# Performance work log

Measured on AMD Instinct MI355X. Metric: run time of the kernel, lower is better.

## Reference

```python
import jax, jax.numpy as jnp
import numpy as np
import math

B, F, N, EMB, H, NC, L = 16, 60, 512, 128, 4, 27, 2
EPS = 1e-5


def _ln(x, g, b):
    m = x.mean(-1, keepdims=True)
    v = ((x - m) ** 2).mean(-1, keepdims=True)
    return (x - m) / jnp.sqrt(v + EPS) * g + b


def _bn(x, g, b):
    # BatchNorm1d in training mode: batch statistics over dim 0
    m = x.mean(0)
    v = ((x - m) ** 2).mean(0)
    return (x - m) / jnp.sqrt(v + EPS) * g + b


def _pos_encoding(S, D):
    pos = jnp.arange(S, dtype=jnp.float32)[:, None]
    div = jnp.exp(jnp.arange(0, D, 2, dtype=jnp.float32) * (-math.log(10000.0) / D))
    ang = pos * div  # [S, D/2]
    return jnp.stack([jnp.sin(ang), jnp.cos(ang)], axis=-1).reshape(S, D)


def setup_inputs():
    key = jax.random.key(0)
    ks = jax.random.split(key, 16)
    rn = lambda i, shape, s: (jax.random.normal(ks[i], shape) * s).astype(jnp.float32)
    z = lambda *shape: jnp.zeros(shape, jnp.float32)
    o = lambda *shape: jnp.ones(shape, jnp.float32)
    return {
        "x": jax.random.normal(ks[0], (B, F, N, 3), dtype=jnp.float32),
        "frame_length": jax.random.randint(ks[1], (B,), 1, F + 1, dtype=jnp.int32),
        # PointNet encoder (shared per-point MLP 3->64->128->EMB, max-pool)
        "enc_w1": rn(2, (3, 64), 0.3), "enc_b1": z(64),
        "enc_w2": rn(3, (64, 128), 0.1), "enc_b2": z(128),
        "enc_w3": rn(4, (128, EMB), 0.1), "enc_b3": z(EMB),
        "cls_token": rn(5, (1, 1, EMB), 0.02), "cls_pos": rn(6, (1, 1, EMB), 0.02),
        # 2-layer post-norm TransformerEncoder (d=128, h=4, ff=256)
        "in_w": rn(7, (L, 3 * EMB, EMB), 0.05), "in_b": z(L, 3 * EMB),
        "out_w": rn(8, (L, EMB, EMB), 0.05), "out_b": z(L, EMB),
        "ln1_g": o(L, EMB), "ln1_b": z(L, EMB),
        "ff1_w": rn(9, (L, 256, EMB), 0.05), "ff1_b": z(L, 256),
        "ff2_w": rn(10, (L, EMB, 256), 0.05), "ff2_b": z(L, EMB),
        "ln2_g": o(L, EMB), "ln2_b": z(L, EMB),
        # MLP head (weights stored [in, out])
        "fc1_w": rn(11, (2 * EMB, 128), 0.05), "fc1_b": z(128),
        "bn1_g": o(128), "bn1_b": z(128),
        "fc15_w": rn(12, (128, 64), 0.05), "fc15_b": z(64),
        "bn15_g": o(64), "bn15_b": z(64),
        "fc2_w": rn(13, (64, 32), 0.05), "fc2_b": z(32),
        "bn2_g": o(32), "bn2_b": z(32),
        "fc_w": rn(14, (32, NC), 0.05), "fc_b": z(NC),
    }


def _forward(x, frame_length, enc_w1, enc_b1, enc_w2, enc_b2, enc_w3, enc_b3,
             cls_token, cls_pos, in_w, in_b, out_w, out_b, ln1_g, ln1_b,
             ff1_w, ff1_b, ff2_w, ff2_b, ln2_g, ln2_b,
             fc1_w, fc1_b, bn1_g, bn1_b, fc15_w, fc15_b, bn15_g, bn15_b,
             fc2_w, fc2_b, bn2_g, bn2_b, fc_w, fc_b):
    dh = EMB // H
    # --- per-frame PointNet encoder, vectorized over (B, F) ---
    # (replaces the ragged Python loop; padded frames are masked to zero below,
    #  exactly matching y = zeros(...) filled only for valid frames)
    h = jax.nn.relu(jnp.einsum('bfnc,cd->bfnd', x, enc_w1) + enc_b1)
    h = jax.nn.relu(h @ enc_w2 + enc_b2)
    h = h @ enc_w3 + enc_b3
    y = h.max(axis=2)  # [B, F, EMB]
    valid = (jnp.arange(F)[None, :] < frame_length[:, None])  # [B, F]
    y = jnp.where(valid[..., None], y, 0.0)

    # --- cls token + sinusoidal positions ---
    pe = _pos_encoding(F, EMB)[None]  # [1, F, EMB]
    y = jnp.concatenate([jnp.broadcast_to(cls_token, (B, 1, EMB)), y], axis=1)
    pos = jnp.concatenate([cls_pos, pe], axis=1)
    y = y + pos  # [B, F+1, EMB]

    S = F + 1
    kpm = jnp.arange(S)[None, :] >= (frame_length + 1)[:, None]  # True = pad
    bias = jnp.where(kpm, -1e9, 0.0)[:, None, None, :]  # [B,1,1,S]

    for l in range(L):
        qkv = y @ in_w[l].T + in_b[l]  # [B,S,3*EMB]
        q, k, v = jnp.split(qkv, 3, axis=-1)
        q = q.reshape(B, S, H, dh).transpose(0, 2, 1, 3)
        k = k.reshape(B, S, H, dh).transpose(0, 2, 1, 3)
        v = v.reshape(B, S, H, dh).transpose(0, 2, 1, 3)
        scores = jnp.einsum('bhqd,bhkd->bhqk', q, k) / math.sqrt(dh) + bias
        attn = jax.nn.softmax(scores, axis=-1)
        o = jnp.einsum('bhqk,bhkd->bhqd', attn, v).transpose(0, 2, 1, 3).reshape(B, S, EMB)
        y = _ln(y + (o @ out_w[l].T + out_b[l]), ln1_g[l], ln1_b[l])
        ff = jax.nn.relu(y @ ff1_w[l].T + ff1_b[l]) @ ff2_w[l].T + ff2_b[l]
        y = _ln(y + ff, ln2_g[l], ln2_b[l])

    # --- ragged gather: cls output + last valid frame output ---
    z1 = y[:, 0, :]
    z2 = y[jnp.arange(B), frame_length]  # position frame_length[i] (cls offset)
    zc = jnp.concatenate([z1, z2], axis=1)  # [B, 2*EMB]

    lrelu = lambda t: jax.nn.leaky_relu(t, negative_slope=0.2)
    y1 = lrelu(_bn(zc @ fc1_w + fc1_b, bn1_g, bn1_b))
    y1 = lrelu(_bn(y1 @ fc15_w + fc15_b, bn15_g, bn15_b))
    y1 = lrelu(_bn(y1 @ fc2_w + fc2_b, bn2_g, bn2_b))
    return y1 @ fc_w + fc_b  # [B, NC]


def reference(x, frame_length, enc_w1, enc_b1, enc_w2, enc_b2, enc_w3, enc_b3,
              cls_token, cls_pos, in_w, in_b, out_w, out_b, ln1_g, ln1_b,
              ff1_w, ff1_b, ff2_w, ff2_b, ln2_g, ln2_b,
              fc1_w, fc1_b, bn1_g, bn1_b, fc15_w, fc15_b, bn15_g, bn15_b,
              fc2_w, fc2_b, bn2_g, bn2_b, fc_w, fc_b):
    return _forward(x, frame_length, enc_w1, enc_b1, enc_w2, enc_b2, enc_w3, enc_b3,
                    cls_token, cls_pos, in_w, in_b, out_w, out_b, ln1_g, ln1_b,
                    ff1_w, ff1_b, ff2_w, ff2_b, ln2_g, ln2_b,
                    fc1_w, fc1_b, bn1_g, bn1_b, fc15_w, fc15_b, bn15_g, bn15_b,
                    fc2_w, fc2_b, bn2_g, bn2_b, fc_w, fc_b)
```

## Files before the change

### kernel.cpp

```cpp
#include <hip/hip_runtime.h>
#include <math.h>

#define SS 61
#define EPSV 1e-5f

typedef __attribute__((ext_vector_type(8))) short bf16x8;
typedef __attribute__((ext_vector_type(4))) short s16x4;
typedef __attribute__((ext_vector_type(4))) float f32x4;

__device__ __forceinline__ short f2bf(float f){
  return __builtin_bit_cast(short, (__bf16)f);
}
__device__ __forceinline__ float bf2f(short s){
  unsigned u = ((unsigned)(unsigned short)s) << 16;
  return __builtin_bit_cast(float, u);
}
__device__ __forceinline__ bf16x8 pack8(f32x4 lo, f32x4 hi){
  bf16x8 r;
  r[0]=f2bf(lo[0]); r[1]=f2bf(lo[1]); r[2]=f2bf(lo[2]); r[3]=f2bf(lo[3]);
  r[4]=f2bf(hi[0]); r[5]=f2bf(hi[1]); r[6]=f2bf(hi[2]); r[7]=f2bf(hi[3]);
  return r;
}
__device__ __forceinline__ s16x4 pack4(f32x4 v){
  s16x4 r; r[0]=f2bf(v[0]); r[1]=f2bf(v[1]); r[2]=f2bf(v[2]); r[3]=f2bf(v[3]); return r;
}
#define YI(t,d) (((t)<<7) + ((d) ^ (((t)&7)<<2)))
#define OI(t,e) (((t)<<7) + ((e) ^ (((t)&7)<<2)))
#define FI(t,e) (((t)<<8) + ((e) ^ (((t)&7)<<2)))
#define VI(k,d) (((k)<<5) + ((d) ^ (((k)&7)<<2)))

__global__ __launch_bounds__(256) void prep_kernel(
    const float* __restrict__ ew1, const float* __restrict__ eb1,
    const float* __restrict__ ew2, const float* __restrict__ ew3,
    const float* __restrict__ in_w, const float* __restrict__ ow,
    const float* __restrict__ f1w, const float* __restrict__ f2w,
    const float* __restrict__ fc1w, const float* __restrict__ fc15w,
    const float* __restrict__ fc2w, const float* __restrict__ fcw,
    unsigned short* __restrict__ wbf)
{
  int s = blockIdx.x * 256 + threadIdx.x;
  int i = s & 7, lane = (s >> 3) & 63, frag = s >> 9;
  int c = lane & 15, g = lane >> 4;
  int sig = 16 * (i >> 2) + 4 * g + (i & 3);
  unsigned short outv;
  if (frag < 8) {
    int mt = frag & 3;
    float base = (sig < 3) ? ew1[sig * 64 + 16 * mt + c]
               : (sig == 3 ? eb1[16 * mt + c] : 0.f);
    short hv = f2bf(base);
    if (frag < 4) outv = (unsigned short)hv;
    else { float rv = base - bf2f(hv); outv = (unsigned short)f2bf(rv); }
  } else if (frag < 24) {
    int f = frag - 8; int mt = f >> 1, ks = f & 1;
    outv = (unsigned short)f2bf(ew2[(32 * ks + sig) * 128 + 16 * mt + c]);
  } else if (frag < 56) {
    int f = frag - 24; int mt = f >> 2, ks = f & 3;
    outv = (unsigned short)f2bf(ew3[(32 * ks + sig) * 128 + 16 * mt + c]);
  } else if (frag < 568) {
    int f = frag - 56; int l = f >> 8; f &= 255;
    float v;
    if (f < 96) { int tq = f >> 2, ks = f & 3;
      v = in_w[(size_t)l * 49152 + (size_t)(16 * tq + c) * 128 + 32 * ks + sig]; }
    else if (f < 128) { int f3 = f - 96; int t = f3 >> 2, ks = f3 & 3;
      v = ow[(size_t)l * 16384 + (size_t)(16 * t + c) * 128 + 32 * ks + sig]; }
    else if (f < 192) { int f3 = f - 128; int t = f3 >> 2, ks = f3 & 3;
      v = f1w[(size_t)l * 32768 + (size_t)(16 * t + c) * 128 + 32 * ks + sig]; }
    else { int f3 = f - 192; int t = f3 >> 3, ks = f3 & 7;
      v = f2w[(size_t)l * 32768 + (size_t)(16 * t + c) * 256 + 32 * ks + sig]; }
    outv = (unsigned short)f2bf(v);
  } else {
    int f = frag - 568;
    float v; int hl;
    if (f < 128) { hl = f >> 6; int f6 = f & 63; int mt = f6 >> 3, ks = f6 & 7;
      v = fc1w[(32 * ks + sig) * 128 + 16 * mt + c]; }
    else if (f < 160) { int f2_ = f - 128; hl = f2_ >> 4; int f4 = f2_ & 15; int mt = f4 >> 2, ks = f4 & 3;
      v = fc15w[(32 * ks + sig) * 64 + 16 * mt + c]; }
    else if (f < 168) { int f2_ = f - 160; hl = f2_ >> 2; int f4 = f2_ & 3; int mt = f4 >> 1, ks = f4 & 1;
      v = fc2w[(32 * ks + sig) * 32 + 16 * mt + c]; }
    else { int f2_ = f - 168; hl = f2_ >> 1; int mt = f2_ & 1; int m = 16 * mt + c;
      v = (m < 27) ? fcw[sig * 27 + m] : 0.f; }
    short hv = f2bf(v);
    outv = hl ? (unsigned short)f2bf(v - bf2f(hv)) : (unsigned short)hv;
  }
  wbf[s] = outv;
}

__global__ __launch_bounds__(256, 1) void enc_kernel(
    const float* __restrict__ x,
    const float* __restrict__ eb2, const float* __restrict__ eb3,
    const unsigned short* __restrict__ wbf,
    float* __restrict__ ymax)
{
  const int tid = threadIdx.x, lane = tid & 63, wv = tid >> 6;
  const int c = lane & 15, g = lane >> 4;
  const int frame = blockIdx.x * 4 + wv;
  const bf16x8* wf = (const bf16x8*)wbf;

  bf16x8 A1h[4], A1l[4];
#pragma unroll
  for (int mt = 0; mt < 4; mt++) { A1h[mt] = wf[mt * 64 + lane]; A1l[mt] = wf[(4 + mt) * 64 + lane]; }
  bf16x8 A2f[8][2];
#pragma unroll
  for (int mt = 0; mt < 8; mt++)
#pragma unroll
    for (int ks = 0; ks < 2; ks++) A2f[mt][ks] = wf[(8 + mt * 2 + ks) * 64 + lane];
  bf16x8 A3f[8][4];
#pragma unroll
  for (int mt = 0; mt < 8; mt++)
#pragma unroll
    for (int ks = 0; ks < 4; ks++) A3f[mt][ks] = wf[(24 + mt * 4 + ks) * 64 + lane];
  f32x4 b2v[8];
#pragma unroll
  for (int mt = 0; mt < 8; mt++) b2v[mt] = *(const f32x4*)(eb2 + 16 * mt + 4 * g);

  f32x4 pool[8];
#pragma unroll
  for (int mt = 0; mt < 8; mt++) pool[mt] = {-1e30f, -1e30f, -1e30f, -1e30f};

  const float* xf = x + (size_t)frame * 1536;
  float nx[2][3];
#pragma unroll
  for (int nt = 0; nt < 2; nt++) {
    const float* xp = xf + (16 * nt + c) * 3;
    nx[nt][0] = xp[0]; nx[nt][1] = xp[1]; nx[nt][2] = xp[2];
  }

  for (int t = 0; t < 16; t++) {
    float cx[2][3];
#pragma unroll
    for (int nt = 0; nt < 2; nt++) {
      cx[nt][0] = nx[nt][0]; cx[nt][1] = nx[nt][1]; cx[nt][2] = nx[nt][2];
    }
    if (t < 15) {
#pragma unroll
      for (int nt = 0; nt < 2; nt++) {
        const float* xp = xf + ((t + 1) * 32 + 16 * nt + c) * 3;
        nx[nt][0] = xp[0]; nx[nt][1] = xp[1]; nx[nt][2] = xp[2];
      }
    }
#pragma unroll
    for (int nt = 0; nt < 2; nt++) {
      bf16x8 bxh = {0,0,0,0,0,0,0,0}, bxl = {0,0,0,0,0,0,0,0};
      if (g == 0) {
        short h0 = f2bf(cx[nt][0]), h1_ = f2bf(cx[nt][1]), h2_ = f2bf(cx[nt][2]);
        bxh[0] = h0; bxh[1] = h1_; bxh[2] = h2_; bxh[3] = (short)0x3F80;
        bxl[0] = f2bf(cx[nt][0] - bf2f(h0));
        bxl[1] = f2bf(cx[nt][1] - bf2f(h1_));
        bxl[2] = f2bf(cx[nt][2] - bf2f(h2_));
      }
      f32x4 d1[4];
#pragma unroll
      for (int mt = 0; mt < 4; mt++) {
        f32x4 a = {0.f, 0.f, 0.f, 0.f};
        a = __builtin_amdgcn_mfma_f32_16x16x32_bf16(A1h[mt], bxh, a, 0, 0, 0);
        a = __builtin_amdgcn_mfma_f32_16x16x32_bf16(A1h[mt], bxl, a, 0, 0, 0);
        a = __builtin_amdgcn_mfma_f32_16x16x32_bf16(A1l[mt], bxh, a, 0, 0, 0);
        d1[mt] = a;
      }
      bf16x8 B2[2];
#pragma unroll
      for (int ks = 0; ks < 2; ks++) {
        bf16x8 r;
#pragma unroll
        for (int i = 0; i < 8; i++)
          r[i] = f2bf(fmaxf(d1[2 * ks + (i >> 2)][i & 3], 0.f));
        B2[ks] = r;
      }
      f32x4 acc2[8];
#pragma unroll
      for (int mt = 0; mt < 8; mt++) {
        f32x4 a = b2v[mt];
        a = __builtin_amdgcn_mfma_f32_16x16x32_bf16(A2f[mt][0], B2[0], a, 0, 0, 0);
        a = __builtin_amdgcn_mfma_f32_16x16x32_bf16(A2f[mt][1], B2[1], a, 0, 0, 0);
        acc2[mt] = a;
      }
      bf16x8 B3[4];
#pragma unroll
      for (int ks = 0; ks < 4; ks++) {
        bf16x8 r;
#pragma unroll
        for (int i = 0; i < 8; i++)
          r[i] = f2bf(fmaxf(acc2[2 * ks + (i >> 2)][i & 3], 0.f));
        B3[ks] = r;
      }
#pragma unroll
      for (int mt = 0; mt < 8; mt++) {
        f32x4 a = {0.f, 0.f, 0.f, 0.f};
        a = __builtin_amdgcn_mfma_f32_16x16x32_bf16(A3f[mt][0], B3[0], a, 0, 0, 0);
        a = __builtin_amdgcn_mfma_f32_16x16x32_bf16(A3f[mt][1], B3[1], a, 0, 0, 0);
        a = __builtin_amdgcn_mfma_f32_16x16x32_bf16(A3f[mt][2], B3[2], a, 0, 0, 0);
        a = __builtin_amdgcn_mfma_f32_16x16x32_bf16(A3f[mt][3], B3[3], a, 0, 0, 0);
#pragma unroll
        for (int r = 0; r < 4; r++) pool[mt][r] = fmaxf(pool[mt][r], a[r]);
      }
    }
  }

#pragma unroll
  for (int mt = 0; mt < 8; mt++)
#pragma unroll
    for (int r = 0; r < 4; r++) {
      float v = pool[mt][r];
      v = fmaxf(v, __shfl_xor(v, 1, 64));
      v = fmaxf(v, __shfl_xor(v, 2, 64));
      v = fmaxf(v, __shfl_xor(v, 4, 64));
      v = fmaxf(v, __shfl_xor(v, 8, 64));
      pool[mt][r] = v;
    }
  if (c == 0) {
#pragma unroll
    for (int mt = 0; mt < 8; mt++)
#pragma unroll
      for (int r = 0; r < 4; r++) {
        const int ch = 16 * mt + 4 * g + r;
        ymax[(size_t)frame * 128 + ch] = pool[mt][r] + eb3[ch];
      }
  }
}

__global__ __launch_bounds__(512, 1) void xformer_kernel(
    const float* __restrict__ ymax, const int* __restrict__ fl,
    const float* __restrict__ ctok, const float* __restrict__ cpos,
    const unsigned short* __restrict__ wbf,
    const float* __restrict__ in_b, const float* __restrict__ ob,
    const float* __restrict__ l1g, const float* __restrict__ l1b,
    const float* __restrict__ f1b, const float* __restrict__ f2b,
    const float* __restrict__ l2g, const float* __restrict__ l2b,
    float* __restrict__ zbuf)
{
  __shared__ __align__(16) float ylds[64 * 128];
  __shared__ __align__(16) unsigned short ubuf[64 * 256];
  __shared__ __align__(16) unsigned short kq4[2][8][4][64][4];
  const int b = blockIdx.x, tid = threadIdx.x;
  const int w8 = tid >> 6, lane = tid & 63, c = lane & 15, g = lane >> 4;
  const int h = w8 >> 1, sub = w8 & 1;
  const int flb = fl[b];
  const float scl = 0.17677669529663687f;

  for (int it = 0; it < 16; it++) {
    int idx = it * 512 + tid;
    int t = idx >> 7, d = idx & 127;
    float v;
    if (t == 0) v = ctok[d] + cpos[d];
    else if (t <= 60) {
      int f = t - 1;
      float ym = (f < flb) ? ymax[(size_t)(b * 60 + f) * 128 + d] : 0.f;
      float dv = __expf((float)(d & ~1) * (-0.07195578416f));
      float ang = (float)f * dv;
      v = ym + ((d & 1) ? __cosf(ang) : __sinf(ang));
    } else v = 0.f;
    ylds[YI(t, d)] = v;
  }
  __syncthreads();

  for (int l = 0; l < 2; l++) {
    const unsigned short* WL = wbf + 28672 + (size_t)l * 131072;
    const bf16x8* wq  = (const bf16x8*)WL;
    const bf16x8* wo  = (const bf16x8*)(WL + 49152);
    const bf16x8* w1p = (const bf16x8*)(WL + 65536);
    const bf16x8* w2p = (const bf16x8*)(WL + 98304);
    unsigned short* vb = ubuf + 8192 + h * 2048;

    {
      bf16x8 yB[4][4];
#pragma unroll
      for (int nt = 0; nt < 4; nt++)
#pragma unroll
        for (int ks = 0; ks < 4; ks++) {
          f32x4 lo = *(const f32x4*)&ylds[YI(16 * nt + c, 32 * ks + 4 * g)];
          f32x4 hi = *(const f32x4*)&ylds[YI(16 * nt + c, 32 * ks + 16 + 4 * g)];
          yB[nt][ks] = pack8(lo, hi);
        }
#pragma unroll
      for (int p = 0; p < 3; p++) {
        const int tq = p * 8 + w8;
        bf16x8 Af[4];
#pragma unroll
        for (int ks = 0; ks < 4; ks++) Af[ks] = wq[(tq * 4 + ks) * 64 + lane];
        f32x4 bias = *(const f32x4*)(in_b + l * 384 + p * 128 + 16 * w8 + 4 * g);
        f32x4 acc[4];
#pragma unroll
        for (int nt = 0; nt < 4; nt++) acc[nt] = bias;
#pragma unroll
        for (int ks = 0; ks < 4; ks++)
#pragma unroll
          for (int nt = 0; nt < 4; nt++)
            acc[nt] = __builtin_amdgcn_mfma_f32_16x16x32_bf16(Af[ks], yB[nt][ks], acc[nt], 0, 0, 0);
        if (p == 2) {
#pragma unroll
          for (int nt = 0; nt < 4; nt++)
            *(s16x4*)&vb[VI(16 * nt + c, 16 * sub + 4 * g)] = pack4(acc[nt]);
        } else {
#pragma unroll
          for (int nt = 0; nt < 4; nt++) {
            f32x4 sv = acc[nt];
            if (p == 0) sv = sv * scl;
            *(s16x4*)&kq4[p][w8][nt][lane][0] = pack4(sv);
          }
        }
      }
    }
    __syncthreads();

    {
      bf16x8 Ak[4], Bq2[2];
#pragma unroll
      for (int kt = 0; kt < 4; kt++) {
        s16x4 lo = *(const s16x4*)&kq4[1][2 * h][kt][lane][0];
        s16x4 hi = *(const s16x4*)&kq4[1][2 * h + 1][kt][lane][0];
        Ak[kt] = __builtin_shufflevector(lo, hi, 0, 1, 2, 3, 4, 5, 6, 7);
      }
#pragma unroll
      for (int j = 0; j < 2; j++) {
        s16x4 lo = *(const s16x4*)&kq4[0][2 * h][2 * sub + j][lane][0];
        s16x4 hi = *(const s16x4*)&kq4[0][2 * h + 1][2 * sub + j][lane][0];
        Bq2[j] = __builtin_shufflevector(lo, hi, 0, 1, 2, 3, 4, 5, 6, 7);
      }
      f32x4 St[4][2];
#pragma unroll
      for (int kt = 0; kt < 4; kt++)
#pragma unroll
        for (int j = 0; j < 2; j++) {
          f32x4 z = {0.f, 0.f, 0.f, 0.f};
          St[kt][j] = __builtin_amdgcn_mfma_f32_16x16x32_bf16(Ak[kt], Bq2[j], z, 0, 0, 0);
        }
#pragma unroll
      for (int j = 0; j < 2; j++) {
        float m = -1e30f;
#pragma unroll
        for (int kt = 0; kt < 4; kt++)
#pragma unroll
          for (int r = 0; r < 4; r++) {
            const int kp = 16 * kt + 4 * g + r;
            float s = St[kt][j][r];
            s = (kp > flb) ? -1e30f : s;
            St[kt][j][r] = s;
            m = fmaxf(m, s);
          }
        m = fmaxf(m, __shfl_xor(m, 16, 64));
        m = fmaxf(m, __shfl_xor(m, 32, 64));
        float sum = 0.f;
#pragma unroll
        for (int kt = 0; kt < 4; kt++)
#pragma unroll
          for (int r = 0; r < 4; r++) {
            float p = __expf(St[kt][j][r] - m);
            St[kt][j][r] = p;
            sum += p;
          }
        sum += __shfl_xor(sum, 16, 64);
        sum += __shfl_xor(sum, 32, 64);
        const float inv = 1.f / sum;
#pragma unroll
        for (int kt = 0; kt < 4; kt++)
#pragma unroll
          for (int r = 0; r < 4; r++) St[kt][j][r] *= inv;
      }
      bf16x8 Bp[2][2];
#pragma unroll
      for (int j = 0; j < 2; j++)
#pragma unroll
        for (int ks = 0; ks < 2; ks++) {
          bf16x8 r;
#pragma unroll
          for (int i = 0; i < 8; i++) r[i] = f2bf(St[2 * ks + (i >> 2)][j][i & 3]);
          Bp[j][ks] = r;
        }
      bf16x8 Av[2][2];
#pragma unroll
      for (int dt = 0; dt < 2; dt++)
#pragma unroll
        for (int ks = 0; ks < 2; ks++) {
          bf16x8 r;
#pragma unroll
          for (int i = 0; i < 8; i++) {
            const int kp = 32 * ks + 16 * (i >> 2) + 4 * g + (i & 3);
            r[i] = (short)vb[VI(kp, 16 * dt + c)];
          }
          Av[dt][ks] = r;
        }
#pragma unroll
      for (int dt = 0; dt < 2; dt++)
#pragma unroll
        for (int j = 0; j < 2; j++) {
          f32x4 z = {0.f, 0.f, 0.f, 0.f};
          z = __builtin_amdgcn_mfma_f32_16x16x32_bf16(Av[dt][0], Bp[j][0], z, 0, 0, 0);
          z = __builtin_amdgcn_mfma_f32_16x16x32_bf16(Av[dt][1], Bp[j][1], z, 0, 0, 0);
          *(s16x4*)&ubuf[OI(16 * (2 * sub + j) + c, 32 * h + 16 * dt + 4 * g)] = pack4(z);
        }
    }
    __syncthreads();

    {
      bf16x8 Bo[4][4];
#pragma unroll
      for (int nt = 0; nt < 4; nt++)
#pragma unroll
        for (int ks = 0; ks < 4; ks++) {
          s16x4 lo = *(const s16x4*)&ubuf[OI(16 * nt + c, 32 * ks + 4 * g)];
          s16x4 hi = *(const s16x4*)&ubuf[OI(16 * nt + c, 32 * ks + 16 + 4 * g)];
          Bo[nt][ks] = __builtin_shufflevector(lo, hi, 0, 1, 2, 3, 4, 5, 6, 7);
        }
      const int j0 = 16 * w8;
      bf16x8 Af[4];
#pragma unroll
      for (int ks = 0; ks < 4; ks++) Af[ks] = wo[(w8 * 4 + ks) * 64 + lane];
      f32x4 bias = *(const f32x4*)(ob + l * 128 + j0 + 4 * g);
      f32x4 acc[4];
#pragma unroll
      for (int nt = 0; nt < 4; nt++) acc[nt] = bias;
#pragma unroll
      for (int ks = 0; ks < 4; ks++)
#pragma unroll
        for (int nt = 0; nt < 4; nt++)
          acc[nt] = __builtin_amdgcn_mfma_f32_16x16x32_bf16(Af[ks], Bo[nt][ks], acc[nt], 0, 0, 0);
#pragma unroll
      for (int nt = 0; nt < 4; nt++) {
        float* yp = &ylds[YI(16 * nt + c, j0 + 4 * g)];
        *(f32x4*)yp = *(const f32x4*)yp + acc[nt];
      }
    }
    __syncthreads();
    {
      const int t = 8 * w8 + (lane >> 3);
      const int s = lane & 7;
      f32x4 vv[4];
      float s1 = 0.f, s2 = 0.f;
#pragma unroll
      for (int k = 0; k < 4; k++) {
        vv[k] = *(const f32x4*)&ylds[YI(t, s * 16 + 4 * k)];
#pragma unroll
        for (int r = 0; r < 4; r++) { s1 += vv[k][r]; s2 = fmaf(vv[k][r], vv[k][r], s2); }
      }
      s1 += __shfl_xor(s1, 1, 64); s1 += __shfl_xor(s1, 2, 64); s1 += __shfl_xor(s1, 4, 64);
      s2 += __shfl_xor(s2, 1, 64); s2 += __shfl_xor(s2, 2, 64); s2 += __shfl_xor(s2, 4, 64);
      const float mean = s1 * 0.0078125f;
      const float var  = s2 * 0.0078125f - mean * mean;
      const float inv  = rsqrtf(var + EPSV);
#pragma unroll
      for (int k = 0; k < 4; k++) {
        f32x4 gg = *(const f32x4*)(l1g + l * 128 + s * 16 + 4 * k);
        f32x4 bb = *(const f32x4*)(l1b + l * 128 + s * 16 + 4 * k);
        f32x4 o;
#pragma unroll
        for (int r = 0; r < 4; r++) o[r] = (vv[k][r] - mean) * inv * gg[r] + bb[r];
        *(f32x4*)&ylds[YI(t, s * 16 + 4 * k)] = o;
      }
    }
    __syncthreads();

    {
      bf16x8 yB[4][4];
#pragma unroll
      for (int nt = 0; nt < 4; nt++)
#pragma unroll
        for (int ks = 0; ks < 4; ks++) {
          f32x4 lo = *(const f32x4*)&ylds[YI(16 * nt + c, 32 * ks + 4 * g)];
          f32x4 hi = *(const f32x4*)&ylds[YI(16 * nt + c, 32 * ks + 16 + 4 * g)];
          yB[nt][ks] = pack8(lo, hi);
        }
#pragma unroll
      for (int half = 0; half < 2; half++) {
        const int t16 = 8 * half + w8;
        bf16x8 Af[4];
#pragma unroll
        for (int ks = 0; ks < 4; ks++) Af[ks] = w1p[(t16 * 4 + ks) * 64 + lane];
        f32x4 bias = *(const f32x4*)(f1b + l * 256 + 16 * t16 + 4 * g);
        f32x4 acc[4];
#pragma unroll
        for (int nt = 0; nt < 4; nt++) acc[nt] = bias;
#pragma unroll
        for (int ks = 0; ks < 4; ks++)
#pragma unroll
          for (int nt = 0; nt < 4; nt++)
            acc[nt] = __builtin_amdgcn_mfma_f32_16x16x32_bf16(Af[ks], yB[nt][ks], acc[nt], 0, 0, 0);
#pragma unroll
        for (int nt = 0; nt < 4; nt++) {
          f32x4 rl;
#pragma unroll
          for (int r = 0; r < 4; r++) rl[r] = fmaxf(acc[nt][r], 0.f);
          *(s16x4*)&ubuf[FI(16 * nt + c, 16 * t16 + 4 * g)] = pack4(rl);
        }
      }
    }
    __syncthreads();
    {
      f32x4 acc[4];
      f32x4 bias = *(const f32x4*)(f2b + l * 128 + 16 * w8 + 4 * g);
#pragma unroll
      for (int nt = 0; nt < 4; nt++) acc[nt] = bias;
#pragma unroll
      for (int ks = 0; ks < 8; ks++) {
        bf16x8 Af = w2p[(w8 * 8 + ks) * 64 + lane];
        bf16x8 Bf[4];
#pragma unroll
        for (int nt = 0; nt < 4; nt++) {
          s16x4 lo = *(const s16x4*)&ubuf[FI(16 * nt + c, 32 * ks + 4 * g)];
          s16x4 hi = *(const s16x4*)&ubuf[FI(16 * nt + c, 32 * ks + 16 + 4 * g)];
          Bf[nt] = __builtin_shufflevector(lo, hi, 0, 1, 2, 3, 4, 5, 6, 7);
        }
#pragma unroll
        for (int nt = 0; nt < 4; nt++)
          acc[nt] = __builtin_amdgcn_mfma_f32_16x16x32_bf16(Af, Bf[nt], acc[nt], 0, 0, 0);
      }
#pragma unroll
      for (int nt = 0; nt < 4; nt++) {
        float* yp = &ylds[YI(16 * nt + c, 16 * w8 + 4 * g)];
        *(f32x4*)yp = *(const f32x4*)yp + acc[nt];
      }
    }
    __syncthreads();
    {
      const int t = 8 * w8 + (lane >> 3);
      const int s = lane & 7;
      f32x4 vv[4];
      float s1 = 0.f, s2 = 0.f;
#pragma unroll
      for (int k = 0; k < 4; k++) {
        vv[k] = *(const f32x4*)&ylds[YI(t, s * 16 + 4 * k)];
#pragma unroll
        for (int r = 0; r < 4; r++) { s1 += vv[k][r]; s2 = fmaf(vv[k][r], vv[k][r], s2); }
      }
      s1 += __shfl_xor(s1, 1, 64); s1 += __shfl_xor(s1, 2, 64); s1 += __shfl_xor(s1, 4, 64);
      s2 += __shfl_xor(s2, 1, 64); s2 += __shfl_xor(s2, 2, 64); s2 += __shfl_xor(s2, 4, 64);
      const float mean = s1 * 0.0078125f;
      const float var  = s2 * 0.0078125f - mean * mean;
      const float inv  = rsqrtf(var + EPSV);
#pragma unroll
      for (int k = 0; k < 4; k++) {
        f32x4 gg = *(const f32x4*)(l2g + l * 128 + s * 16 + 4 * k);
        f32x4 bb = *(const f32x4*)(l2b + l * 128 + s * 16 + 4 * k);
        f32x4 o;
#pragma unroll
        for (int r = 0; r < 4; r++) o[r] = (vv[k][r] - mean) * inv * gg[r] + bb[r];
        *(f32x4*)&ylds[YI(t, s * 16 + 4 * k)] = o;
      }
    }
    __syncthreads();
  }

  if (tid < 256) {
    const int d = tid;
    float v = (d < 128) ? ylds[YI(0, d)] : ylds[YI(flb, d - 128)];
    zbuf[d * 16 + b] = v;
  }
}

__device__ __forceinline__ void buildB(const float* src, int ks, int g, int c,
                                       bf16x8& bh, bf16x8& bl){
#pragma unroll
  for (int i = 0; i < 8; i++) {
    int k = 32 * ks + 16 * (i >> 2) + 4 * g + (i & 3);
    float v = src[k * 16 + c];
    short hv = f2bf(v);
    bh[i] = hv; bl[i] = f2bf(v - bf2f(hv));
  }
}
__device__ __forceinline__ void bn_lrelu_store(f32x4 acc, int ch0, int c,
    const float* __restrict__ gg, const float* __restrict__ bb, float* dst){
#pragma unroll
  for (int r = 0; r < 4; r++) {
    float v = acc[r];
    float s1 = v, s2 = v * v;
    s1 += __shfl_xor(s1, 1, 64); s2 += __shfl_xor(s2, 1, 64);
    s1 += __shfl_xor(s1, 2, 64); s2 += __shfl_xor(s2, 2, 64);
    s1 += __shfl_xor(s1, 4, 64); s2 += __shfl_xor(s2, 4, 64);
    s1 += __shfl_xor(s1, 8, 64); s2 += __shfl_xor(s2, 8, 64);
    const float m = s1 * (1.f / 16.f);
    const float var = s2 * (1.f / 16.f) - m * m;
    const float scl = gg[ch0 + r] / sqrtf(var + EPSV);
    const float sh = bb[ch0 + r] - m * scl;
    float o = v * scl + sh;
    o = (o > 0.f) ? o : 0.2f * o;
    dst[(ch0 + r) * 16 + c] = o;
  }
}

__global__ __launch_bounds__(256, 1) void head_kernel(
    const float* __restrict__ zt, const unsigned short* __restrict__ wbf,
    const float* __restrict__ fc1b, const float* __restrict__ bn1g, const float* __restrict__ bn1b,
    const float* __restrict__ fc15b, const float* __restrict__ bn15g, const float* __restrict__ bn15b,
    const float* __restrict__ fc2b, const float* __restrict__ bn2g, const float* __restrict__ bn2b,
    const float* __restrict__ fcb, float* __restrict__ out)
{
  __shared__ float zs[256 * 16];
  __shared__ float t1s[128 * 16];
  __shared__ float t15s[64 * 16];
  __shared__ float t2s[32 * 16];
  const int tid = threadIdx.x, lane = tid & 63, wv = tid >> 6;
  const int c = lane & 15, g = lane >> 4;
  const bf16x8* wf = (const bf16x8*)wbf;

  for (int idx = tid; idx < 4096; idx += 256) zs[idx] = zt[idx];
  __syncthreads();

  {
    f32x4 acc[2];
#pragma unroll
    for (int j = 0; j < 2; j++) {
      const int ch0 = 16 * (2 * wv + j) + 4 * g;
      f32x4 a;
#pragma unroll
      for (int r = 0; r < 4; r++) a[r] = fc1b[ch0 + r];
      acc[j] = a;
    }
#pragma unroll
    for (int ks = 0; ks < 8; ks++) {
      bf16x8 bh, bl; buildB(zs, ks, g, c, bh, bl);
#pragma unroll
      for (int j = 0; j < 2; j++) {
        const int mt = 2 * wv + j;
        bf16x8 Ah = wf[(568 + mt * 8 + ks) * 64 + lane];
        bf16x8 Al = wf[(632 + mt * 8 + ks) * 64 + lane];
        acc[j] = __builtin_amdgcn_mfma_f32_16x16x32_bf16(Ah, bh, acc[j], 0, 0, 0);
        acc[j] = __builtin_amdgcn_mfma_f32_16x16x32_bf16(Ah, bl, acc[j], 0, 0, 0);
        acc[j] = __builtin_amdgcn_mfma_f32_16x16x32_bf16(Al, bh, acc[j], 0, 0, 0);
      }
    }
#pragma unroll
    for (int j = 0; j < 2; j++)
      bn_lrelu_store(acc[j], 16 * (2 * wv + j) + 4 * g, c, bn1g, bn1b, t1s);
  }
  __syncthreads();

  {
    const int ch0 = 16 * wv + 4 * g;
    f32x4 a;
#pragma unroll
    for (int r = 0; r < 4; r++) a[r] = fc15b[ch0 + r];
#pragma unroll
    for (int ks = 0; ks < 4; ks++) {
      bf16x8 bh, bl; buildB(t1s, ks, g, c, bh, bl);
      bf16x8 Ah = wf[(696 + wv * 4 + ks) * 64 + lane];
      bf16x8 Al = wf[(712 + wv * 4 + ks) * 64 + lane];
      a = __builtin_amdgcn_mfma_f32_16x16x32_bf16(Ah, bh, a, 0, 0, 0);
      a = __builtin_amdgcn_mfma_f32_16x16x32_bf16(Ah, bl, a, 0, 0, 0);
      a = __builtin_amdgcn_mfma_f32_16x16x32_bf16(Al, bh, a, 0, 0, 0);
    }
    bn_lrelu_store(a, ch0, c, bn15g, bn15b, t15s);
  }
  __syncthreads();

  if (wv < 2) {
    const int ch0 = 16 * wv + 4 * g;
    f32x4 a;
#pragma unroll
    for (int r = 0; r < 4; r++) a[r] = fc2b[ch0 + r];
#pragma unroll
    for (int ks = 0; ks < 2; ks++) {
      bf16x8 bh, bl; buildB(t15s, ks, g, c, bh, bl);
      bf16x8 Ah = wf[(728 + wv * 2 + ks) * 64 + lane];
      bf16x8 Al = wf[(732 + wv * 2 + ks) * 64 + lane];
      a = __builtin_amdgcn_mfma_f32_16x16x32_bf16(Ah, bh, a, 0, 0, 0);
      a = __builtin_amdgcn_mfma_f32_16x16x32_bf16(Ah, bl, a, 0, 0, 0);
      a = __builtin_amdgcn_mfma_f32_16x16x32_bf16(Al, bh, a, 0, 0, 0);
    }
    bn_lrelu_store(a, ch0, c, bn2g, bn2b, t2s);
  }
  __syncthreads();

  if (wv < 2) {
    f32x4 a;
#pragma unroll
    for (int r = 0; r < 4; r++) {
      const int ch = 16 * wv + 4 * g + r;
      a[r] = (ch < 27) ? fcb[ch] : 0.f;
    }
    bf16x8 bh, bl; buildB(t2s, 0, g, c, bh, bl);
    bf16x8 Ah = wf[(736 + wv) * 64 + lane];
    bf16x8 Al = wf[(738 + wv) * 64 + lane];
    a = __builtin_amdgcn_mfma_f32_16x16x32_bf16(Ah, bh, a, 0, 0, 0);
    a = __builtin_amdgcn_mfma_f32_16x16x32_bf16(Ah, bl, a, 0, 0, 0);
    a = __builtin_amdgcn_mfma_f32_16x16x32_bf16(Al, bh, a, 0, 0, 0);
#pragma unroll
    for (int r = 0; r < 4; r++) {
      const int ch = 16 * wv + 4 * g + r;
      if (ch < 27) out[c * 27 + ch] = a[r];
    }
  }
}

extern "C" void kernel_launch(void* const* d_in, const int* in_sizes, int n_in,
                              void* d_out, int out_size, void* d_ws, size_t ws_size,
                              hipStream_t stream)
{
  const float* x    = (const float*)d_in[0];
  const int*   fl   = (const int*)d_in[1];
  const float* ew1  = (const float*)d_in[2];  const float* eb1 = (const float*)d_in[3];
  const float* ew2  = (const float*)d_in[4];  const float* eb2 = (const float*)d_in[5];
  const float* ew3  = (const float*)d_in[6];  const float* eb3 = (const float*)d_in[7];
  const float* ctok = (const float*)d_in[8];  const float* cpos = (const float*)d_in[9];
  const float* in_w = (const float*)d_in[10]; const float* in_b = (const float*)d_in[11];
  const float* ow   = (const float*)d_in[12]; const float* ob   = (const float*)d_in[13];
  const float* l1g  = (const float*)d_in[14]; const float* l1b  = (const float*)d_in[15];
  const float* f1w  = (const float*)d_in[16]; const float* f1b  = (const float*)d_in[17];
  const float* f2w  = (const float*)d_in[18]; const float* f2b  = (const float*)d_in[19];
  const float* l2g  = (const float*)d_in[20]; const float* l2b  = (const float*)d_in[21];
  const float* fc1w = (const float*)d_in[22]; const float* fc1b = (const float*)d_in[23];
  const float* bn1g = (const float*)d_in[24]; const float* bn1b = (const float*)d_in[25];
  const float* fc15w= (const float*)d_in[26]; const float* fc15b= (const float*)d_in[27];
  const float* bn15g= (const float*)d_in[28]; const float* bn15b= (const float*)d_in[29];
  const float* fc2w = (const float*)d_in[30]; const float* fc2b = (const float*)d_in[31];
  const float* bn2g = (const float*)d_in[32]; const float* bn2b = (const float*)d_in[33];
  const float* fcw  = (const float*)d_in[34]; const float* fcb  = (const float*)d_in[35];
  float* out = (float*)d_out;

  char* w = (char*)d_ws;
  float* ymax = (float*)w;
  float* zbuf = (float*)(w + 491520);
  unsigned short* wbf = (unsigned short*)(w + 507904);

  prep_kernel<<<1480, 256, 0, stream>>>(ew1, eb1, ew2, ew3, in_w, ow, f1w, f2w,
                                        fc1w, fc15w, fc2w, fcw, wbf);
  enc_kernel<<<240, 256, 0, stream>>>(x, eb2, eb3, wbf, ymax);
  xformer_kernel<<<16, 512, 0, stream>>>(ymax, fl, ctok, cpos, wbf, in_b, ob,
                                         l1g, l1b, f1b, f2b, l2g, l2b, zbuf);
  head_kernel<<<1, 256, 0, stream>>>(zbuf, wbf, fc1b, bn1g, bn1b,
                                     fc15b, bn15g, bn15b, fc2b, bn2g, bn2b, fcb, out);
}
```

Measured before the change: 81.79 us.

## Split encoder into producer/consumer wave pairs with double-buffered LDS handoff

```diff
diff --git a/kernel.cpp b/kernel.cpp
--- a/kernel.cpp
+++ b/kernel.cpp
@@ -85,136 +85,162 @@
   wbf[s] = outv;
 }
 
-__global__ __launch_bounds__(256, 1) void enc_kernel(
+__global__ __launch_bounds__(512, 2) void enc_kernel(
     const float* __restrict__ x,
     const float* __restrict__ eb2, const float* __restrict__ eb3,
     const unsigned short* __restrict__ wbf,
     float* __restrict__ ymax)
 {
+  __shared__ __align__(16) unsigned short h2x[4][2][2][32][64];
   const int tid = threadIdx.x, lane = tid & 63, wv = tid >> 6;
   const int c = lane & 15, g = lane >> 4;
-  const int frame = blockIdx.x * 4 + wv;
+  const int pair = wv >> 1, role = wv & 1;
+  const int frame = blockIdx.x * 4 + pair;
   const bf16x8* wf = (const bf16x8*)wbf;
-
-  bf16x8 A1h[4], A1l[4];
-#pragma unroll
-  for (int mt = 0; mt < 4; mt++) { A1h[mt] = wf[mt * 64 + lane]; A1l[mt] = wf[(4 + mt) * 64 + lane]; }
-  bf16x8 A2f[8][2];
-#pragma unroll
-  for (int mt = 0; mt < 8; mt++)
-#pragma unroll
-    for (int ks = 0; ks < 2; ks++) A2f[mt][ks] = wf[(8 + mt * 2 + ks) * 64 + lane];
-  bf16x8 A3f[8][4];
-#pragma unroll
-  for (int mt = 0; mt < 8; mt++)
-#pragma unroll
-    for (int ks = 0; ks < 4; ks++) A3f[mt][ks] = wf[(24 + mt * 4 + ks) * 64 + lane];
-  f32x4 b2v[8];
-#pragma unroll
-  for (int mt = 0; mt < 8; mt++) b2v[mt] = *(const f32x4*)(eb2 + 16 * mt + 4 * g);
-
-  f32x4 pool[8];
-#pragma unroll
-  for (int mt = 0; mt < 8; mt++) pool[mt] = {-1e30f, -1e30f, -1e30f, -1e30f};
-
-  const float* xf = x + (size_t)frame * 1536;
-  float nx[2][3];
-#pragma unroll
-  for (int nt = 0; nt < 2; nt++) {
-    const float* xp = xf + (16 * nt + c) * 3;
-    nx[nt][0] = xp[0]; nx[nt][1] = xp[1]; nx[nt][2] = xp[2];
-  }
-
-  for (int t = 0; t < 16; t++) {
-    float cx[2][3];
+  const int swap8 = c >> 3;
+
+  if (role == 0) {
+    bf16x8 A1h[4], A1l[4];
+#pragma unroll
+    for (int mt = 0; mt < 4; mt++) { A1h[mt] = wf[mt * 64 + lane]; A1l[mt] = wf[(4 + mt) * 64 + lane]; }
+    bf16x8 A2f[8][2];
+#pragma unroll
+    for (int mt = 0; mt < 8; mt++)
+#pragma unroll
+      for (int ks = 0; ks < 2; ks++) A2f[mt][ks] = wf[(8 + mt * 2 + ks) * 64 + lane];
+    f32x4 b2v[8];
+#pragma unroll
+    for (int mt = 0; mt < 8; mt++) b2v[mt] = *(const f32x4*)(eb2 + 16 * mt + 4 * g);
+
+    const float* xf = x + (size_t)frame * 1536;
+    float nx[2][3];
 #pragma unroll
     for (int nt = 0; nt < 2; nt++) {
-      cx[nt][0] = nx[nt][0]; cx[nt][1] = nx[nt][1]; cx[nt][2] = nx[nt][2];
-    }
-    if (t < 15) {
+      const float* xp = xf + (16 * nt + c) * 3;
+      nx[nt][0] = xp[0]; nx[nt][1] = xp[1]; nx[nt][2] = xp[2];
+    }
+
+    for (int t = 0; t <= 16; t++) {
+      __syncthreads();
+      if (t >= 16) continue;
+      float cx[2][3];
 #pragma unroll
       for (int nt = 0; nt < 2; nt++) {
-        const float* xp = xf + ((t + 1) * 32 + 16 * nt + c) * 3;
-        nx[nt][0] = xp[0]; nx[nt][1] = xp[1]; nx[nt][2] = xp[2];
-      }
-    }
-#pragma unroll
-    for (int nt = 0; nt < 2; nt++) {
-      bf16x8 bxh = {0,0,0,0,0,0,0,0}, bxl = {0,0,0,0,0,0,0,0};
-      if (g == 0) {
-        short h0 = f2bf(cx[nt][0]), h1_ = f2bf(cx[nt][1]), h2_ = f2bf(cx[nt][2]);
-        bxh[0] = h0; bxh[1] = h1_; bxh[2] = h2_; bxh[3] = (short)0x3F80;
-        bxl[0] = f2bf(cx[nt][0] - bf2f(h0));
-        bxl[1] = f2bf(cx[nt][1] - bf2f(h1_));
-        bxl[2] = f2bf(cx[nt][2] - bf2f(h2_));
-      }
-      f32x4 d1[4];
-#pragma unroll
-      for (int mt = 0; mt < 4; mt++) {
-        f32x4 a = {0.f, 0.f, 0.f, 0.f};
-        a = __builtin_amdgcn_mfma_f32_16x16x32_bf16(A1h[mt], bxh, a, 0, 0, 0);
-        a = __builtin_amdgcn_mfma_f32_16x16x32_bf16(A1h[mt], bxl, a, 0, 0, 0);
-        a = __builtin_amdgcn_mfma_f32_16x16x32_bf16(A1l[mt], bxh, a, 0, 0, 0);
-        d1[mt] = a;
-      }
-      bf16x8 B2[2];
-#pragma unroll
-      for (int ks = 0; ks < 2; ks++) {
-        bf16x8 r;
-#pragma unroll
-        for (int i = 0; i < 8; i++)
-          r[i] = f2bf(fmaxf(d1[2 * ks + (i >> 2)][i & 3], 0.f));
-        B2[ks] = r;
-      }
-      f32x4 acc2[8];
-#pragma unroll
-      for (int mt = 0; mt < 8; mt++) {
-        f32x4 a = b2v[mt];
-        a = __builtin_amdgcn_mfma_f32_16x16x32_bf16(A2f[mt][0], B2[0], a, 0, 0, 0);
-        a = __builtin_amdgcn_mfma_f32_16x16x32_bf16(A2f[mt][1], B2[1], a, 0, 0, 0);
-        acc2[mt] = a;
-      }
-      bf16x8 B3[4];
-#pragma unroll
-      for (int ks = 0; ks < 4; ks++) {
-        bf16x8 r;
-#pragma unroll
-        for (int i = 0; i < 8; i++)
-          r[i] = f2bf(fmaxf(acc2[2 * ks + (i >> 2)][i & 3], 0.f));
-        B3[ks] = r;
-      }
-#pragma unroll
-      for (int mt = 0; mt < 8; mt++) {
-        f32x4 a = {0.f, 0.f, 0.f, 0.f};
-        a = __builtin_amdgcn_mfma_f32_16x16x32_bf16(A3f[mt][0], B3[0], a, 0, 0, 0);
-        a = __builtin_amdgcn_mfma_f32_16x16x32_bf16(A3f[mt][1], B3[1], a, 0, 0, 0);
-        a = __builtin_amdgcn_mfma_f32_16x16x32_bf16(A3f[mt][2], B3[2], a, 0, 0, 0);
-        a = __builtin_amdgcn_mfma_f32_16x16x32_bf16(A3f[mt][3], B3[3], a, 0, 0, 0);
-#pragma unroll
-        for (int r = 0; r < 4; r++) pool[mt][r] = fmaxf(pool[mt][r], a[r]);
-      }
-    }
-  }
-
-#pragma unroll
-  for (int mt = 0; mt < 8; mt++)
-#pragma unroll
-    for (int r = 0; r < 4; r++) {
-      float v = pool[mt][r];
-      v = fmaxf(v, __shfl_xor(v, 1, 64));
-      v = fmaxf(v, __shfl_xor(v, 2, 64));
-      v = fmaxf(v, __shfl_xor(v, 4, 64));
-      v = fmaxf(v, __shfl_xor(v, 8, 64));
-      pool[mt][r] = v;
-    }
-  if (c == 0) {
+        cx[nt][0] = nx[nt][0]; cx[nt][1] = nx[nt][1]; cx[nt][2] = nx[nt][2];
+      }
+      if (t < 15) {
+#pragma unroll
+        for (int nt = 0; nt < 2; nt++) {
+          const float* xp = xf + ((t + 1) * 32 + 16 * nt + c) * 3;
+          nx[nt][0] = xp[0]; nx[nt][1] = xp[1]; nx[nt][2] = xp[2];
+        }
+      }
+#pragma unroll
+      for (int nt = 0; nt < 2; nt++) {
+        bf16x8 bxh = {0,0,0,0,0,0,0,0}, bxl = {0,0,0,0,0,0,0,0};
+        if (g == 0) {
+          short h0 = f2bf(cx[nt][0]), h1_ = f2bf(cx[nt][1]), h2_ = f2bf(cx[nt][2]);
+          bxh[0] = h0; bxh[1] = h1_; bxh[2] = h2_; bxh[3] = (short)0x3F80;
+          bxl[0] = f2bf(cx[nt][0] - bf2f(h0));
+          bxl[1] = f2bf(cx[nt][1] - bf2f(h1_));
+          bxl[2] = f2bf(cx[nt][2] - bf2f(h2_));
+        }
+        f32x4 d1[4];
+#pragma unroll
+        for (int mt = 0; mt < 4; mt++) {
+          f32x4 a = {0.f, 0.f, 0.f, 0.f};
+          a = __builtin_amdgcn_mfma_f32_16x16x32_bf16(A1h[mt], bxh, a, 0, 0, 0);
+          a = __builtin_amdgcn_mfma_f32_16x16x32_bf16(A1h[mt], bxl, a, 0, 0, 0);
+          a = __builtin_amdgcn_mfma_f32_16x16x32_bf16(A1l[mt], bxh, a, 0, 0, 0);
+          d1[mt] = a;
+        }
+        bf16x8 B2[2];
+#pragma unroll
+        for (int ks = 0; ks < 2; ks++) {
+          bf16x8 r;
+#pragma unroll
+          for (int i = 0; i < 8; i++)
+            r[i] = f2bf(fmaxf(d1[2 * ks + (i >> 2)][i & 3], 0.f));
+          B2[ks] = r;
+        }
+        const int pt = 16 * nt + c;
+#pragma unroll
+        for (int mt = 0; mt < 8; mt++) {
+          f32x4 a = b2v[mt];
+          a = __builtin_amdgcn_mfma_f32_16x16x32_bf16(A2f[mt][0], B2[0], a, 0, 0, 0);
+          a = __builtin_amdgcn_mfma_f32_16x16x32_bf16(A2f[mt][1], B2[1], a, 0, 0, 0);
+          f32x4 rl;
+#pragma unroll
+          for (int r = 0; r < 4; r++) rl[r] = fmaxf(a[r], 0.f);
+          const int half = mt >> 2, j = mt & 3;
+          unsigned short* hb = &h2x[pair][t & 1][half][0][0];
+          const int idx2 = ((j >> 1) * 32 + g * 8 + (j & 1) * 4) * 2;
+          const int off = (idx2 ^ ((pt & 7) << 4)) ^ (swap8 << 3);
+          *(s16x4*)((char*)hb + pt * 128 + off) = pack4(rl);
+        }
+      }
+    }
+  } else {
+    bf16x8 A3f[8][4];
 #pragma unroll
     for (int mt = 0; mt < 8; mt++)
 #pragma unroll
+      for (int ks = 0; ks < 4; ks++) A3f[mt][ks] = wf[(24 + mt * 4 + ks) * 64 + lane];
+    f32x4 pool[8];
+#pragma unroll
+    for (int mt = 0; mt < 8; mt++) pool[mt] = {-1e30f, -1e30f, -1e30f, -1e30f};
+
+    for (int t = 0; t <= 16; t++) {
+      __syncthreads();
+      if (t == 0) continue;
+      const int tb = (t - 1) & 1;
+#pragma unroll
+      for (int nt = 0; nt < 2; nt++) {
+        const int pt = 16 * nt + c;
+        bf16x8 Bx[4];
+#pragma unroll
+        for (int half = 0; half < 2; half++)
+#pragma unroll
+          for (int ksl = 0; ksl < 2; ksl++) {
+            const unsigned short* hb = &h2x[pair][tb][half][0][0];
+            const int off = (64 * ksl + 16 * g) ^ ((pt & 7) << 4);
+            bf16x8 v = *(const bf16x8*)((const char*)hb + pt * 128 + off);
+            bf16x8 vs = __builtin_shufflevector(v, v, 4, 5, 6, 7, 0, 1, 2, 3);
+            Bx[2 * half + ksl] = swap8 ? vs : v;
+          }
+#pragma unroll
+        for (int mt = 0; mt < 8; mt++) {
+          f32x4 a = {0.f, 0.f, 0.f, 0.f};
+          a = __builtin_amdgcn_mfma_f32_16x16x32_bf16(A3f[mt][0], Bx[0], a, 0, 0, 0);
+          a = __builtin_amdgcn_mfma_f32_16x16x32_bf16(A3f[mt][1], Bx[1], a, 0, 0, 0);
+          a = __builtin_amdgcn_mfma_f32_16x16x32_bf16(A3f[mt][2], Bx[2], a, 0, 0, 0);
+          a = __builtin_amdgcn_mfma_f32_16x16x32_bf16(A3f[mt][3], Bx[3], a, 0, 0, 0);
+#pragma unroll
+          for (int r = 0; r < 4; r++) pool[mt][r] = fmaxf(pool[mt][r], a[r]);
+        }
+      }
+    }
+
+#pragma unroll
+    for (int mt = 0; mt < 8; mt++)
+#pragma unroll
       for (int r = 0; r < 4; r++) {
-        const int ch = 16 * mt + 4 * g + r;
-        ymax[(size_t)frame * 128 + ch] = pool[mt][r] + eb3[ch];
-      }
+        float v = pool[mt][r];
+        v = fmaxf(v, __shfl_xor(v, 1, 64));
+        v = fmaxf(v, __shfl_xor(v, 2, 64));
+        v = fmaxf(v, __shfl_xor(v, 4, 64));
+        v = fmaxf(v, __shfl_xor(v, 8, 64));
+        pool[mt][r] = v;
+      }
+    if (c == 0) {
+#pragma unroll
+      for (int mt = 0; mt < 8; mt++)
+#pragma unroll
+        for (int r = 0; r < 4; r++) {
+          const int ch = 16 * mt + 4 * g + r;
+          ymax[(size_t)frame * 128 + ch] = pool[mt][r] + eb3[ch];
+        }
+    }
   }
 }
 
@@ -712,7 +738,7 @@
 
   prep_kernel<<<1480, 256, 0, stream>>>(ew1, eb1, ew2, ew3, in_w, ow, f1w, f2w,
                                         fc1w, fc15w, fc2w, fcw, wbf);
-  enc_kernel<<<240, 256, 0, stream>>>(x, eb2, eb3, wbf, ymax);
+  enc_kernel<<<240, 512, 0, stream>>>(x, eb2, eb3, wbf, ymax);
   xformer_kernel<<<16, 512, 0, stream>>>(ymax, fl, ctok, cpos, wbf, in_b, ob,
                                          l1g, l1b, f1b, f2b, l2g, l2b, zbuf);
   head_kernel<<<1, 256, 0, stream>>>(zbuf, wbf, fc1b, bn1g, bn1b,
```

New measurement: 83.57 us. 1.02x slower.
